# Kernel optimization log

Measured on AMD Instinct MI355X. Metric: run time of the kernel, lower is better.

## Reference

```python
import jax, jax.numpy as jnp
import numpy as np

N_EMBD = 128
N_HEADS = 8
HEAD_SIZE = N_EMBD // N_HEADS  # 16
EPS = 1e-5


def _layernorm(x, g, b):
    m = jnp.mean(x, axis=-1, keepdims=True)
    v = jnp.mean(jnp.square(x - m), axis=-1, keepdims=True)
    return (x - m) * jax.lax.rsqrt(v + EPS) * g + b


def setup_inputs() -> dict:
    key = jax.random.key(0)
    ks = jax.random.split(key, 12)
    B, T, D, H, HS = 16, 1024, N_EMBD, N_HEADS, HEAD_SIZE
    s = 1.0 / np.sqrt(D)
    inp = {
        "x": jax.random.normal(ks[0], (B, T, D), jnp.float32),
        # per-head QKV projections (stacked over heads; matches ModuleList of Linear(D, HS))
        "Wq": jax.random.uniform(ks[1], (H, D, HS), jnp.float32, -s, s),
        "bq": jnp.zeros((H, HS), jnp.float32),
        "Wk": jax.random.uniform(ks[2], (H, D, HS), jnp.float32, -s, s),
        "bk": jnp.zeros((H, HS), jnp.float32),
        "Wv": jax.random.uniform(ks[3], (H, D, HS), jnp.float32, -s, s),
        "bv": jnp.zeros((H, HS), jnp.float32),
        "Wp": jax.random.uniform(ks[4], (H * HS, D), jnp.float32, -s, s),
        "bp": jnp.zeros((D,), jnp.float32),
        "W1": jax.random.uniform(ks[5], (D, 4 * D), jnp.float32, -s, s),
        "b1": jnp.zeros((4 * D,), jnp.float32),
        "W2": jax.random.uniform(ks[6], (4 * D, D), jnp.float32, -1.0 / np.sqrt(4 * D), 1.0 / np.sqrt(4 * D)),
        "b2": jnp.zeros((D,), jnp.float32),
        "g1": jnp.ones((D,), jnp.float32),
        "be1": jnp.zeros((D,), jnp.float32),
        "g2": jnp.ones((D,), jnp.float32),
        "be2": jnp.zeros((D,), jnp.float32),
    }
    return inp


def reference(x, Wq, bq, Wk, bk, Wv, bv, Wp, bp, W1, b1, W2, b2, g1, be1, g2, be2):
    B, T, D = x.shape
    # batched per-head projections: [B,T,D] x [H,D,HS] -> [B,H,T,HS]
    q = jnp.einsum("btd,hds->bhts", x, Wq) + bq[None, :, None, :]
    k = jnp.einsum("btd,hds->bhts", x, Wk) + bk[None, :, None, :]
    v = jnp.einsum("btd,hds->bhts", x, Wv) + bv[None, :, None, :]
    scores = jnp.einsum("bhts,bhus->bhtu", q, k) / np.sqrt(HEAD_SIZE).astype(np.float32)
    tril = jnp.tril(jnp.ones((T, T), x.dtype))
    # faithful to source: multiplicative + additive mask (not -inf where)
    scores = scores * tril - 1e12 * (1.0 - tril)
    attn = jax.nn.softmax(scores, axis=-1)
    out = jnp.einsum("bhtu,bhus->bhts", attn, v)  # [B,H,T,HS]
    # concat heads in head order -> [B,T,H*HS]
    out = out.transpose(0, 2, 1, 3).reshape(B, T, -1)
    attn_out = out @ Wp + bp
    x = _layernorm(attn_out + x, g1, be1)
    h = jax.nn.gelu(x @ W1 + b1, approximate=False) @ W2 + b2
    x = _layernorm(h + x, g2, be2)
    return x
```

## Files before the change

### kernel.cpp

```cpp
#include <hip/hip_runtime.h>
#include <hip/hip_bf16.h>
#include <math.h>

constexpr int NB  = 16;
constexpr int NT  = 1024;
constexpr int ND  = 128;
constexpr int NH  = 8;
constexpr int NHS = 16;
constexpr int NDH = 512;
constexpr long NBT = (long)NB * NT;

typedef __attribute__((ext_vector_type(8))) short short8;
typedef __attribute__((ext_vector_type(4))) float f32x4;
typedef __attribute__((ext_vector_type(4))) unsigned short us4;

__device__ __forceinline__ unsigned short f2bf(float f) {
    __hip_bfloat16 h = __float2bfloat16(f);
    return *(unsigned short*)&h;
}

__device__ __forceinline__ short8 cvt8(const float* p) {
    const float4 f0 = *(const float4*)p;
    const float4 f1 = *(const float4*)(p + 4);
    union { short8 s; __hip_bfloat162 h[4]; } u;
    u.h[0] = __float22bfloat162_rn(make_float2(f0.x, f0.y));
    u.h[1] = __float22bfloat162_rn(make_float2(f0.z, f0.w));
    u.h[2] = __float22bfloat162_rn(make_float2(f1.x, f1.y));
    u.h[3] = __float22bfloat162_rn(make_float2(f1.z, f1.w));
    return u.s;
}

__device__ __forceinline__ float fast_gelu(float y) {
    const float t = y * y;
    const float u = __builtin_fmaf(y * 0.044715f, t, y);
    const float e = __builtin_amdgcn_exp2f(u * -2.302118131f);
    return y * __builtin_amdgcn_rcpf(1.0f + e);
}

__global__ __launch_bounds__(256) void k_prep(
    const float* __restrict__ Wq, const float* __restrict__ Wk,
    const float* __restrict__ Wv, __hip_bfloat16* __restrict__ Wqkvt)
{
    const int blk = blockIdx.x, tid = threadIdx.x;
    const int i0 = blk * 1024 + tid * 4;
    const int n = i0 >> 7, d0 = i0 & 127;
    const int sec = n >> 7, m = n & 127;
    const float* W = (sec == 0) ? Wq : (sec == 1) ? Wk : Wv;
    const float* src = W + (m >> 4) * 2048 + (m & 15);
    us4 v;
    #pragma unroll
    for (int j = 0; j < 4; ++j) v[j] = f2bf(src[(d0 + j) * 16]);
    *(us4*)((unsigned short*)Wqkvt + i0) = v;
}

__global__ __launch_bounds__(256) void k_qkv(
    const float* __restrict__ x, const __hip_bfloat16* __restrict__ Wqkvt,
    const float* __restrict__ bq, const float* __restrict__ bk,
    const float* __restrict__ bv,
    const float* __restrict__ Wp, const float* __restrict__ W1,
    const float* __restrict__ W2,
    __hip_bfloat16* __restrict__ Wpt, __hip_bfloat16* __restrict__ W1t,
    __hip_bfloat16* __restrict__ W2t,
    __hip_bfloat16* __restrict__ qo, __hip_bfloat16* __restrict__ ko,
    __hip_bfloat16* __restrict__ vo)
{
    __shared__ __align__(16) unsigned short st[32 * 392];
    const int tid = threadIdx.x;

    if (blockIdx.x >= 512) {
        const int blk = blockIdx.x - 512 + 48;
        us4 v;
        if (blk < 64) {
            const int i0 = (blk - 48) * 1024 + tid * 4;
            const int n = i0 >> 7, d0 = i0 & 127;
            #pragma unroll
            for (int j = 0; j < 4; ++j) v[j] = f2bf(Wp[(d0 + j) * 128 + n]);
            *(us4*)((unsigned short*)Wpt + i0) = v;
        } else if (blk < 128) {
            const int i0 = (blk - 64) * 1024 + tid * 4;
            const int n = i0 >> 7, d0 = i0 & 127;
            #pragma unroll
            for (int j = 0; j < 4; ++j) v[j] = f2bf(W1[(d0 + j) * 512 + n]);
            *(us4*)((unsigned short*)W1t + i0) = v;
        } else {
            const int i0 = (blk - 128) * 1024 + tid * 4;
            const int n = i0 >> 9, k0 = i0 & 511;
            #pragma unroll
            for (int j = 0; j < 4; ++j) v[j] = f2bf(W2[(k0 + j) * 128 + n]);
            *(us4*)((unsigned short*)W2t + i0) = v;
        }
        return;
    }

    const int w    = tid >> 6;
    const int lane = tid & 63;
    const int sL   = lane & 15;
    const int quad = lane >> 4;
    const int tok0 = blockIdx.x * 32;

    const unsigned short* W = (const unsigned short*)Wqkvt;

    short8 bx[2][4];
    #pragma unroll
    for (int tt = 0; tt < 2; ++tt)
        #pragma unroll
        for (int ks = 0; ks < 4; ++ks)
            bx[tt][ks] = cvt8(x + (size_t)(tok0 + tt * 16 + sL) * 128 + ks * 32 + quad * 8);

    f32x4 acc[6][2];
    #pragma unroll
    for (int ci = 0; ci < 6; ++ci)
        #pragma unroll
        for (int tt = 0; tt < 2; ++tt)
            acc[ci][tt] = (f32x4){0.f, 0.f, 0.f, 0.f};

    #pragma unroll
    for (int ks = 0; ks < 4; ++ks) {
        short8 aW[6];
        #pragma unroll
        for (int ci = 0; ci < 6; ++ci) {
            const int ct = w * 6 + ci;
            aW[ci] = *(const short8*)(W + (size_t)(ct * 16 + sL) * 128 + ks * 32 + quad * 8);
        }
        #pragma unroll
        for (int ci = 0; ci < 6; ++ci)
            #pragma unroll
            for (int tt = 0; tt < 2; ++tt)
                acc[ci][tt] = __builtin_amdgcn_mfma_f32_16x16x32_bf16(aW[ci], bx[tt][ks], acc[ci][tt], 0, 0, 0);
    }

    const float qscale = 0.3606737602f;
    #pragma unroll
    for (int ci = 0; ci < 6; ++ci) {
        const int ct = w * 6 + ci;
        const int kind = ct >> 3;
        const int ncc = (ct & 7) * 16 + quad * 4;
        const float4 bb = *(const float4*)(((kind == 0) ? bq : (kind == 1) ? bk : bv) + ncc);
        #pragma unroll
        for (int tt = 0; tt < 2; ++tt) {
            us4 v;
            #pragma unroll
            for (int r = 0; r < 4; ++r) {
                float val = acc[ci][tt][r] + ((const float*)&bb)[r];
                if (kind == 0) val *= qscale;
                v[r] = f2bf(val);
            }
            *(us4*)(st + (tt * 16 + sL) * 392 + ct * 16 + quad * 4) = v;
        }
    }
    __syncthreads();

    const int b = tok0 >> 10, tt0 = tok0 & 1023;
    {
        const int h = tid >> 5, tok = tid & 31;
        const unsigned short* sq = st + tok * 392 + h * 16;
        const unsigned short* sk = st + tok * 392 + 128 + h * 16;
        unsigned short* dq = (unsigned short*)qo + ((size_t)(b * 8 + h) * 1024 + tt0 + tok) * 16;
        unsigned short* dk = (unsigned short*)ko + ((size_t)(b * 8 + h) * 1024 + tt0 + tok) * 16;
        *(short8*)dq       = *(const short8*)sq;
        *(short8*)(dq + 8) = *(const short8*)(sq + 8);
        *(short8*)dk       = *(const short8*)sk;
        *(short8*)(dk + 8) = *(const short8*)(sk + 8);
    }
    if (tid < 128) {
        const int h = tid >> 4, s = tid & 15;
        unsigned short tmp[32];
        #pragma unroll
        for (int tok = 0; tok < 32; ++tok)
            tmp[tok] = st[tok * 392 + 256 + h * 16 + s];
        unsigned short* dv = (unsigned short*)vo + ((size_t)(b * 8 + h) * 16 + s) * 1024 + tt0;
        #pragma unroll
        for (int j = 0; j < 4; ++j)
            *(short8*)(dv + j * 8) = *(const short8*)(tmp + j * 8);
    }
}

__global__ __launch_bounds__(256) void k_attn(
    const __hip_bfloat16* __restrict__ qb, const __hip_bfloat16* __restrict__ kb,
    const __hip_bfloat16* __restrict__ vtb, __hip_bfloat16* __restrict__ att)
{
    const int bh   = blockIdx.x & 127;
    const int sub  = blockIdx.x >> 7;
    const int wave = threadIdx.x >> 6;
    const int lane = threadIdx.x & 63;
    const int sL   = lane & 15;
    const int q    = lane >> 4;
    const int b = bh >> 3, h = bh & 7;
    const int tile = sub * 4 + wave;

    const char* qbase = (const char*)qb  + (size_t)bh * NT * NHS * 2;
    const char* kbase = (const char*)kb  + (size_t)bh * NT * NHS * 2;
    const char* vbase = (const char*)vtb + (size_t)bh * NHS * NT * 2;

    const short8 zz = {0,0,0,0,0,0,0,0};

    const int t0 = tile * 16;
    const int tmy = t0 + sL;

    short8 bQ = zz;
    if (q < 2) bQ = *(const short8*)(qbase + (size_t)tmy * 32 + q * 16);

    f32x4 o = {0.f, 0.f, 0.f, 0.f};
    float lp = 0.f;

    const int nch = (t0 + 47) >> 5;
    for (int c = 0; c < nch; ++c) {
        const int u0 = c * 32;
        short8 aK0 = zz, aK1 = zz;
        if (q < 2) {
            aK0 = *(const short8*)(kbase + (size_t)(u0 + sL) * 32 + q * 16);
            aK1 = *(const short8*)(kbase + (size_t)(u0 + 16 + sL) * 32 + q * 16);
        }
        const f32x4 zc = {0.f, 0.f, 0.f, 0.f};
        f32x4 sT0 = __builtin_amdgcn_mfma_f32_16x16x32_bf16(aK0, bQ, zc, 0, 0, 0);
        f32x4 sT1 = __builtin_amdgcn_mfma_f32_16x16x32_bf16(aK1, bQ, zc, 0, 0, 0);

        int pk[4];
        if (u0 + 31 <= t0) {
            #pragma unroll
            for (int r = 0; r < 4; ++r) {
                const float p0 = __builtin_amdgcn_exp2f(sT0[r]);
                const float p1 = __builtin_amdgcn_exp2f(sT1[r]);
                lp += p0 + p1;
                __hip_bfloat162 hh = __float22bfloat162_rn(make_float2(p0, p1));
                pk[r] = *(int*)&hh;
            }
        } else {
            #pragma unroll
            for (int r = 0; r < 4; ++r) {
                const int ua = u0 + 4 * q + r;
                const float e0 = __builtin_amdgcn_exp2f(sT0[r]);
                const float e1 = __builtin_amdgcn_exp2f(sT1[r]);
                const float p0 = (ua      <= tmy) ? e0 : 0.f;
                const float p1 = (ua + 16 <= tmy) ? e1 : 0.f;
                lp += p0 + p1;
                __hip_bfloat162 hh = __float22bfloat162_rn(make_float2(p0, p1));
                pk[r] = *(int*)&hh;
            }
        }

        short8 bP;
        #pragma unroll
        for (int j = 0; j < 8; ++j) {
            const int srcq = ((q & 1) << 1) + (j >> 2);
            const int src  = (srcq << 4) + sL;
            const int g = __shfl(pk[j & 3], src);
            bP[j] = (short)((q < 2) ? (g & 0xffff) : ((unsigned)g >> 16));
        }

        const short8 aV = *(const short8*)(vbase + ((size_t)sL * NT + u0 + q * 8) * 2);
        o = __builtin_amdgcn_mfma_f32_16x16x32_bf16(aV, bP, o, 0, 0, 0);
    }

    float l = lp;
    l += __shfl_xor(l, 16);
    l += __shfl_xor(l, 32);
    const float inv = 1.0f / l;
    us4 res;
    res[0] = f2bf(o[0] * inv); res[1] = f2bf(o[1] * inv);
    res[2] = f2bf(o[2] * inv); res[3] = f2bf(o[3] * inv);
    *(us4*)((unsigned short*)att + ((size_t)b * NT + tmy) * ND + h * NHS + q * 4) = res;
}

__global__ __launch_bounds__(256) void k_tail(
    const __hip_bfloat16* __restrict__ attb, const __hip_bfloat16* __restrict__ Wpt,
    const __hip_bfloat16* __restrict__ W1t, const __hip_bfloat16* __restrict__ W2t,
    const float* __restrict__ x, const float* __restrict__ bp,
    const float* __restrict__ g1, const float* __restrict__ be1,
    const float* __restrict__ b1, const float* __restrict__ b2,
    const float* __restrict__ g2, const float* __restrict__ be2,
    float* __restrict__ out)
{
    __shared__ float ys[32][132];
    __shared__ __align__(16) unsigned short l1b[32 * 136];
    __shared__ __align__(16) unsigned short midb[32 * 528];
    const int w    = threadIdx.x >> 6;
    const int lane = threadIdx.x & 63;
    const int sL   = lane & 15;
    const int quad = lane >> 4;
    const int tok0 = blockIdx.x * 32;

    {
        const unsigned short* A = (const unsigned short*)attb;
        const unsigned short* W = (const unsigned short*)Wpt;
        short8 bfr[2][4];
        #pragma unroll
        for (int tt = 0; tt < 2; ++tt)
            #pragma unroll
            for (int ks = 0; ks < 4; ++ks)
                bfr[tt][ks] = *(const short8*)(A + (size_t)(tok0 + tt * 16 + sL) * 128 + ks * 32 + quad * 8);

        f32x4 acc[2][2];
        #pragma unroll
        for (int ci = 0; ci < 2; ++ci)
            #pragma unroll
            for (int tt = 0; tt < 2; ++tt)
                acc[ci][tt] = (f32x4){0.f, 0.f, 0.f, 0.f};

        #pragma unroll
        for (int ks = 0; ks < 4; ++ks) {
            short8 aW[2];
            #pragma unroll
            for (int ci = 0; ci < 2; ++ci)
                aW[ci] = *(const short8*)(W + (size_t)((w * 2 + ci) * 16 + sL) * 128 + ks * 32 + quad * 8);
            #pragma unroll
            for (int ci = 0; ci < 2; ++ci)
                #pragma unroll
                for (int tt = 0; tt < 2; ++tt)
                    acc[ci][tt] = __builtin_amdgcn_mfma_f32_16x16x32_bf16(aW[ci], bfr[tt][ks], acc[ci][tt], 0, 0, 0);
        }
        #pragma unroll
        for (int ci = 0; ci < 2; ++ci) {
            const int n0 = (w * 2 + ci) * 16 + quad * 4;
            const float4 bb = *(const float4*)(bp + n0);
            #pragma unroll
            for (int tt = 0; tt < 2; ++tt) {
                float4 v;
                v.x = acc[ci][tt][0] + bb.x; v.y = acc[ci][tt][1] + bb.y;
                v.z = acc[ci][tt][2] + bb.z; v.w = acc[ci][tt][3] + bb.w;
                *(float4*)(&ys[tt * 16 + sL][n0]) = v;
            }
        }
    }
    __syncthreads();

    const int tok = threadIdx.x >> 3;
    const int l8  = threadIdx.x & 7;
    const int c0  = l8 * 16;
    {
        float vals[16];
        float s = 0.f, s2 = 0.f;
        #pragma unroll
        for (int ch = 0; ch < 4; ++ch) {
            const float4 ly = *(const float4*)&ys[tok][c0 + ch * 4];
            const float4 gx = *(const float4*)(x + (size_t)(tok0 + tok) * 128 + c0 + ch * 4);
            vals[ch*4+0] = ly.x + gx.x; vals[ch*4+1] = ly.y + gx.y;
            vals[ch*4+2] = ly.z + gx.z; vals[ch*4+3] = ly.w + gx.w;
            #pragma unroll
            for (int j = 0; j < 4; ++j) { s += vals[ch*4+j]; s2 += vals[ch*4+j] * vals[ch*4+j]; }
        }
        #pragma unroll
        for (int off = 1; off <= 4; off <<= 1) {
            s  += __shfl_xor(s, off, 8);
            s2 += __shfl_xor(s2, off, 8);
        }
        const float mean = s * (1.0f / 128.0f);
        const float var  = s2 * (1.0f / 128.0f) - mean * mean;
        const float rstd = rsqrtf(var + 1e-5f);
        #pragma unroll
        for (int ch = 0; ch < 4; ++ch) {
            const float4 gg = *(const float4*)(g1 + c0 + ch * 4);
            const float4 bb = *(const float4*)(be1 + c0 + ch * 4);
            float ln0 = (vals[ch*4+0] - mean) * rstd * gg.x + bb.x;
            float ln1v = (vals[ch*4+1] - mean) * rstd * gg.y + bb.y;
            float ln2v = (vals[ch*4+2] - mean) * rstd * gg.z + bb.z;
            float ln3 = (vals[ch*4+3] - mean) * rstd * gg.w + bb.w;
            ys[tok][c0 + ch*4 + 0] = ln0;
            ys[tok][c0 + ch*4 + 1] = ln1v;
            ys[tok][c0 + ch*4 + 2] = ln2v;
            ys[tok][c0 + ch*4 + 3] = ln3;
            us4 lb;
            lb[0] = f2bf(ln0); lb[1] = f2bf(ln1v); lb[2] = f2bf(ln2v); lb[3] = f2bf(ln3);
            *(us4*)(l1b + tok * 136 + c0 + ch * 4) = lb;
        }
    }
    __syncthreads();

    {
        const unsigned short* W = (const unsigned short*)W1t;
        short8 bl[2][4];
        #pragma unroll
        for (int tt = 0; tt < 2; ++tt)
            #pragma unroll
            for (int ks = 0; ks < 4; ++ks)
                bl[tt][ks] = *(const short8*)(l1b + (tt * 16 + sL) * 136 + ks * 32 + quad * 8);

        f32x4 acc[8][2];
        #pragma unroll
        for (int ci = 0; ci < 8; ++ci)
            #pragma unroll
            for (int tt = 0; tt < 2; ++tt)
                acc[ci][tt] = (f32x4){0.f, 0.f, 0.f, 0.f};

        #pragma unroll
        for (int ks = 0; ks < 4; ++ks) {
            short8 aW[8];
            #pragma unroll
            for (int ci = 0; ci < 8; ++ci)
                aW[ci] = *(const short8*)(W + (size_t)((w * 8 + ci) * 16 + sL) * 128 + ks * 32 + quad * 8);
            #pragma unroll
            for (int ci = 0; ci < 8; ++ci)
                #pragma unroll
                for (int tt = 0; tt < 2; ++tt)
                    acc[ci][tt] = __builtin_amdgcn_mfma_f32_16x16x32_bf16(aW[ci], bl[tt][ks], acc[ci][tt], 0, 0, 0);
        }
        #pragma unroll
        for (int ci = 0; ci < 8; ++ci) {
            const int n0 = (w * 8 + ci) * 16 + quad * 4;
            const float4 bb = *(const float4*)(b1 + n0);
            #pragma unroll
            for (int tt = 0; tt < 2; ++tt) {
                us4 v;
                v[0] = f2bf(fast_gelu(acc[ci][tt][0] + bb.x));
                v[1] = f2bf(fast_gelu(acc[ci][tt][1] + bb.y));
                v[2] = f2bf(fast_gelu(acc[ci][tt][2] + bb.z));
                v[3] = f2bf(fast_gelu(acc[ci][tt][3] + bb.w));
                *(us4*)(midb + (tt * 16 + sL) * 528 + n0) = v;
            }
        }
    }
    __syncthreads();

    f32x4 acc2[2][2];
    #pragma unroll
    for (int ci = 0; ci < 2; ++ci)
        #pragma unroll
        for (int tt = 0; tt < 2; ++tt)
            acc2[ci][tt] = (f32x4){0.f, 0.f, 0.f, 0.f};
    {
        const unsigned short* W = (const unsigned short*)W2t;
        #pragma unroll
        for (int ks = 0; ks < 16; ++ks) {
            short8 bm0 = *(const short8*)(midb + (size_t)sL * 528 + ks * 32 + quad * 8);
            short8 bm1 = *(const short8*)(midb + (size_t)(16 + sL) * 528 + ks * 32 + quad * 8);
            short8 aW0 = *(const short8*)(W + (size_t)((w * 2) * 16 + sL) * 512 + ks * 32 + quad * 8);
            short8 aW1 = *(const short8*)(W + (size_t)((w * 2 + 1) * 16 + sL) * 512 + ks * 32 + quad * 8);
            acc2[0][0] = __builtin_amdgcn_mfma_f32_16x16x32_bf16(aW0, bm0, acc2[0][0], 0, 0, 0);
            acc2[0][1] = __builtin_amdgcn_mfma_f32_16x16x32_bf16(aW0, bm1, acc2[0][1], 0, 0, 0);
            acc2[1][0] = __builtin_amdgcn_mfma_f32_16x16x32_bf16(aW1, bm0, acc2[1][0], 0, 0, 0);
            acc2[1][1] = __builtin_amdgcn_mfma_f32_16x16x32_bf16(aW1, bm1, acc2[1][1], 0, 0, 0);
        }
    }
    __syncthreads();
    float* ys2 = (float*)midb;
    #pragma unroll
    for (int ci = 0; ci < 2; ++ci) {
        const int n0 = (w * 2 + ci) * 16 + quad * 4;
        const float4 bb = *(const float4*)(b2 + n0);
        #pragma unroll
        for (int tt = 0; tt < 2; ++tt) {
            float4 v;
            v.x = acc2[ci][tt][0] + bb.x; v.y = acc2[ci][tt][1] + bb.y;
            v.z = acc2[ci][tt][2] + bb.z; v.w = acc2[ci][tt][3] + bb.w;
            *(float4*)(ys2 + (tt * 16 + sL) * 132 + n0) = v;
        }
    }
    __syncthreads();

    {
        float vals[16];
        float s = 0.f, s2 = 0.f;
        #pragma unroll
        for (int ch = 0; ch < 4; ++ch) {
            const float4 ly = *(const float4*)(ys2 + tok * 132 + c0 + ch * 4);
            const float4 gx = *(const float4*)&ys[tok][c0 + ch * 4];
            vals[ch*4+0] = ly.x + gx.x; vals[ch*4+1] = ly.y + gx.y;
            vals[ch*4+2] = ly.z + gx.z; vals[ch*4+3] = ly.w + gx.w;
            #pragma unroll
            for (int j = 0; j < 4; ++j) { s += vals[ch*4+j]; s2 += vals[ch*4+j] * vals[ch*4+j]; }
        }
        #pragma unroll
        for (int off = 1; off <= 4; off <<= 1) {
            s  += __shfl_xor(s, off, 8);
            s2 += __shfl_xor(s2, off, 8);
        }
        const float mean = s * (1.0f / 128.0f);
        const float var  = s2 * (1.0f / 128.0f) - mean * mean;
        const float rstd = rsqrtf(var + 1e-5f);
        #pragma unroll
        for (int ch = 0; ch < 4; ++ch) {
            const float4 gg = *(const float4*)(g2 + c0 + ch * 4);
            const float4 bb = *(const float4*)(be2 + c0 + ch * 4);
            float4 ln;
            ln.x = (vals[ch*4+0] - mean) * rstd * gg.x + bb.x;
            ln.y = (vals[ch*4+1] - mean) * rstd * gg.y + bb.y;
            ln.z = (vals[ch*4+2] - mean) * rstd * gg.z + bb.z;
            ln.w = (vals[ch*4+3] - mean) * rstd * gg.w + bb.w;
            *(float4*)(out + (size_t)(tok0 + tok) * 128 + c0 + ch * 4) = ln;
        }
    }
}

extern "C" void kernel_launch(void* const* d_in, const int* in_sizes, int n_in,
                              void* d_out, int out_size, void* d_ws, size_t ws_size,
                              hipStream_t stream)
{
    (void)in_sizes; (void)n_in; (void)out_size; (void)ws_size;
    const float* x   = (const float*)d_in[0];
    const float* Wq  = (const float*)d_in[1];
    const float* bq  = (const float*)d_in[2];
    const float* Wk  = (const float*)d_in[3];
    const float* bk  = (const float*)d_in[4];
    const float* Wv  = (const float*)d_in[5];
    const float* bv  = (const float*)d_in[6];
    const float* Wp  = (const float*)d_in[7];
    const float* bp  = (const float*)d_in[8];
    const float* W1  = (const float*)d_in[9];
    const float* b1  = (const float*)d_in[10];
    const float* W2  = (const float*)d_in[11];
    const float* b2  = (const float*)d_in[12];
    const float* g1  = (const float*)d_in[13];
    const float* be1 = (const float*)d_in[14];
    const float* g2  = (const float*)d_in[15];
    const float* be2 = (const float*)d_in[16];
    float* out = (float*)d_out;

    char* wsb = (char*)d_ws;
    __hip_bfloat16* qb   = (__hip_bfloat16*)wsb;
    __hip_bfloat16* kb   = (__hip_bfloat16*)(wsb + (4u  << 20));
    __hip_bfloat16* vtb  = (__hip_bfloat16*)(wsb + (8u  << 20));
    __hip_bfloat16* attb = (__hip_bfloat16*)(wsb + (12u << 20));
    __hip_bfloat16* Wqkvt= (__hip_bfloat16*)(wsb + (16u << 20));
    __hip_bfloat16* Wpt  = (__hip_bfloat16*)(wsb + (16u << 20) + (96u  << 10));
    __hip_bfloat16* W1t  = (__hip_bfloat16*)(wsb + (16u << 20) + (128u << 10));
    __hip_bfloat16* W2t  = (__hip_bfloat16*)(wsb + (16u << 20) + (256u << 10));

    k_prep<<<48,   256, 0, stream>>>(Wq, Wk, Wv, Wqkvt);
    k_qkv <<<656,  256, 0, stream>>>(x, Wqkvt, bq, bk, bv, Wp, W1, W2,
                                     Wpt, W1t, W2t, qb, kb, vtb);
    k_attn<<<2048, 256, 0, stream>>>(qb, kb, vtb, attb);
    k_tail<<<512,  256, 0, stream>>>(attb, Wpt, W1t, W2t, x, bp, g1, be1,
                                     b1, b2, g2, be2, out);
}
```

Baseline: 163.6 us.

## Halve tail kernel token tile to 16 and rebalance causal attention tile mapping

The tail kernel now processes 16 tokens per block instead of 32, doubling the grid to 1024 blocks and shrinking shared memory and accumulator registers. This gives more blocks across the CUs and higher occupancy. The cost is that each block reloads the same weight fragments for half as many tokens, doubling weight traffic from L2. Separately, attention tiles are now assigned as wave*16+sub, so each block mixes short and long causal rows, which is meant to even out per-block work.

```diff
diff --git a/kernel.cpp b/kernel.cpp
--- a/kernel.cpp
+++ b/kernel.cpp
@@ -186,7 +186,7 @@
     const int sL   = lane & 15;
     const int q    = lane >> 4;
     const int b = bh >> 3, h = bh & 7;
-    const int tile = sub * 4 + wave;
+    const int tile = wave * 16 + sub;
 
     const char* qbase = (const char*)qb  + (size_t)bh * NT * NHS * 2;
     const char* kbase = (const char*)kb  + (size_t)bh * NT * NHS * 2;
@@ -271,67 +271,55 @@
     const float* __restrict__ g2, const float* __restrict__ be2,
     float* __restrict__ out)
 {
-    __shared__ float ys[32][132];
-    __shared__ __align__(16) unsigned short l1b[32 * 136];
-    __shared__ __align__(16) unsigned short midb[32 * 528];
+    __shared__ float ys[16][132];
+    __shared__ __align__(16) unsigned short l1b[16 * 136];
+    __shared__ __align__(16) unsigned short midb[16 * 528];
     const int w    = threadIdx.x >> 6;
     const int lane = threadIdx.x & 63;
     const int sL   = lane & 15;
     const int quad = lane >> 4;
-    const int tok0 = blockIdx.x * 32;
+    const int tok0 = blockIdx.x * 16;
 
     {
         const unsigned short* A = (const unsigned short*)attb;
         const unsigned short* W = (const unsigned short*)Wpt;
-        short8 bfr[2][4];
-        #pragma unroll
-        for (int tt = 0; tt < 2; ++tt)
-            #pragma unroll
-            for (int ks = 0; ks < 4; ++ks)
-                bfr[tt][ks] = *(const short8*)(A + (size_t)(tok0 + tt * 16 + sL) * 128 + ks * 32 + quad * 8);
-
-        f32x4 acc[2][2];
-        #pragma unroll
-        for (int ci = 0; ci < 2; ++ci)
-            #pragma unroll
-            for (int tt = 0; tt < 2; ++tt)
-                acc[ci][tt] = (f32x4){0.f, 0.f, 0.f, 0.f};
+        short8 bfr[4];
+        #pragma unroll
+        for (int ks = 0; ks < 4; ++ks)
+            bfr[ks] = *(const short8*)(A + (size_t)(tok0 + sL) * 128 + ks * 32 + quad * 8);
+
+        f32x4 acc[2];
+        acc[0] = (f32x4){0.f, 0.f, 0.f, 0.f};
+        acc[1] = (f32x4){0.f, 0.f, 0.f, 0.f};
 
         #pragma unroll
         for (int ks = 0; ks < 4; ++ks) {
-            short8 aW[2];
-            #pragma unroll
-            for (int ci = 0; ci < 2; ++ci)
-                aW[ci] = *(const short8*)(W + (size_t)((w * 2 + ci) * 16 + sL) * 128 + ks * 32 + quad * 8);
-            #pragma unroll
-            for (int ci = 0; ci < 2; ++ci)
-                #pragma unroll
-                for (int tt = 0; tt < 2; ++tt)
-                    acc[ci][tt] = __builtin_amdgcn_mfma_f32_16x16x32_bf16(aW[ci], bfr[tt][ks], acc[ci][tt], 0, 0, 0);
+            #pragma unroll
+            for (int ci = 0; ci < 2; ++ci) {
+                const short8 aW = *(const short8*)(W + (size_t)((w * 2 + ci) * 16 + sL) * 128 + ks * 32 + quad * 8);
+                acc[ci] = __builtin_amdgcn_mfma_f32_16x16x32_bf16(aW, bfr[ks], acc[ci], 0, 0, 0);
+            }
         }
         #pragma unroll
         for (int ci = 0; ci < 2; ++ci) {
             const int n0 = (w * 2 + ci) * 16 + quad * 4;
             const float4 bb = *(const float4*)(bp + n0);
-            #pragma unroll
-            for (int tt = 0; tt < 2; ++tt) {
-                float4 v;
-                v.x = acc[ci][tt][0] + bb.x; v.y = acc[ci][tt][1] + bb.y;
-                v.z = acc[ci][tt][2] + bb.z; v.w = acc[ci][tt][3] + bb.w;
-                *(float4*)(&ys[tt * 16 + sL][n0]) = v;
-            }
-        }
-    }
-    __syncthreads();
-
-    const int tok = threadIdx.x >> 3;
-    const int l8  = threadIdx.x & 7;
-    const int c0  = l8 * 16;
-    {
-        float vals[16];
+            float4 v;
+            v.x = acc[ci][0] + bb.x; v.y = acc[ci][1] + bb.y;
+            v.z = acc[ci][2] + bb.z; v.w = acc[ci][3] + bb.w;
+            *(float4*)(&ys[sL][n0]) = v;
+        }
+    }
+    __syncthreads();
+
+    const int tok = threadIdx.x >> 4;
+    const int l16 = threadIdx.x & 15;
+    const int c0  = l16 * 8;
+    {
+        float vals[8];
         float s = 0.f, s2 = 0.f;
         #pragma unroll
-        for (int ch = 0; ch < 4; ++ch) {
+        for (int ch = 0; ch < 2; ++ch) {
             const float4 ly = *(const float4*)&ys[tok][c0 + ch * 4];
             const float4 gx = *(const float4*)(x + (size_t)(tok0 + tok) * 128 + c0 + ch * 4);
             vals[ch*4+0] = ly.x + gx.x; vals[ch*4+1] = ly.y + gx.y;
@@ -340,15 +328,15 @@
             for (int j = 0; j < 4; ++j) { s += vals[ch*4+j]; s2 += vals[ch*4+j] * vals[ch*4+j]; }
         }
         #pragma unroll
-        for (int off = 1; off <= 4; off <<= 1) {
-            s  += __shfl_xor(s, off, 8);
-            s2 += __shfl_xor(s2, off, 8);
+        for (int off = 1; off <= 8; off <<= 1) {
+            s  += __shfl_xor(s, off, 16);
+            s2 += __shfl_xor(s2, off, 16);
         }
         const float mean = s * (1.0f / 128.0f);
         const float var  = s2 * (1.0f / 128.0f) - mean * mean;
         const float rstd = rsqrtf(var + 1e-5f);
         #pragma unroll
-        for (int ch = 0; ch < 4; ++ch) {
+        for (int ch = 0; ch < 2; ++ch) {
             const float4 gg = *(const float4*)(g1 + c0 + ch * 4);
             const float4 bb = *(const float4*)(be1 + c0 + ch * 4);
             float ln0 = (vals[ch*4+0] - mean) * rstd * gg.x + bb.x;
@@ -368,67 +356,50 @@
 
     {
         const unsigned short* W = (const unsigned short*)W1t;
-        short8 bl[2][4];
-        #pragma unroll
-        for (int tt = 0; tt < 2; ++tt)
-            #pragma unroll
-            for (int ks = 0; ks < 4; ++ks)
-                bl[tt][ks] = *(const short8*)(l1b + (tt * 16 + sL) * 136 + ks * 32 + quad * 8);
-
-        f32x4 acc[8][2];
+        short8 bl[4];
+        #pragma unroll
+        for (int ks = 0; ks < 4; ++ks)
+            bl[ks] = *(const short8*)(l1b + sL * 136 + ks * 32 + quad * 8);
+
+        f32x4 acc[8];
         #pragma unroll
         for (int ci = 0; ci < 8; ++ci)
-            #pragma unroll
-            for (int tt = 0; tt < 2; ++tt)
-                acc[ci][tt] = (f32x4){0.f, 0.f, 0.f, 0.f};
+            acc[ci] = (f32x4){0.f, 0.f, 0.f, 0.f};
 
         #pragma unroll
         for (int ks = 0; ks < 4; ++ks) {
-            short8 aW[8];
-            #pragma unroll
-            for (int ci = 0; ci < 8; ++ci)
-                aW[ci] = *(const short8*)(W + (size_t)((w * 8 + ci) * 16 + sL) * 128 + ks * 32 + quad * 8);
-            #pragma unroll
-            for (int ci = 0; ci < 8; ++ci)
-                #pragma unroll
-                for (int tt = 0; tt < 2; ++tt)
-                    acc[ci][tt] = __builtin_amdgcn_mfma_f32_16x16x32_bf16(aW[ci], bl[tt][ks], acc[ci][tt], 0, 0, 0);
+            #pragma unroll
+            for (int ci = 0; ci < 8; ++ci) {
+                const short8 aW = *(const short8*)(W + (size_t)((w * 8 + ci) * 16 + sL) * 128 + ks * 32 + quad * 8);
+                acc[ci] = __builtin_amdgcn_mfma_f32_16x16x32_bf16(aW, bl[ks], acc[ci], 0, 0, 0);
+            }
         }
         #pragma unroll
         for (int ci = 0; ci < 8; ++ci) {
             const int n0 = (w * 8 + ci) * 16 + quad * 4;
             const float4 bb = *(const float4*)(b1 + n0);
-            #pragma unroll
-            for (int tt = 0; tt < 2; ++tt) {
-                us4 v;
-                v[0] = f2bf(fast_gelu(acc[ci][tt][0] + bb.x));
-                v[1] = f2bf(fast_gelu(acc[ci][tt][1] + bb.y));
-                v[2] = f2bf(fast_gelu(acc[ci][tt][2] + bb.z));
-                v[3] = f2bf(fast_gelu(acc[ci][tt][3] + bb.w));
-                *(us4*)(midb + (tt * 16 + sL) * 528 + n0) = v;
-            }
-        }
-    }
-    __syncthreads();
-
-    f32x4 acc2[2][2];
-    #pragma unroll
-    for (int ci = 0; ci < 2; ++ci)
-        #pragma unroll
-        for (int tt = 0; tt < 2; ++tt)
-            acc2[ci][tt] = (f32x4){0.f, 0.f, 0.f, 0.f};
+            us4 v;
+            v[0] = f2bf(fast_gelu(acc[ci][0] + bb.x));
+            v[1] = f2bf(fast_gelu(acc[ci][1] + bb.y));
+            v[2] = f2bf(fast_gelu(acc[ci][2] + bb.z));
+            v[3] = f2bf(fast_gelu(acc[ci][3] + bb.w));
+            *(us4*)(midb + sL * 528 + n0) = v;
+        }
+    }
+    __syncthreads();
+
+    f32x4 acc2[2];
+    acc2[0] = (f32x4){0.f, 0.f, 0.f, 0.f};
+    acc2[1] = (f32x4){0.f, 0.f, 0.f, 0.f};
     {
         const unsigned short* W = (const unsigned short*)W2t;
         #pragma unroll
         for (int ks = 0; ks < 16; ++ks) {
-            short8 bm0 = *(const short8*)(midb + (size_t)sL * 528 + ks * 32 + quad * 8);
-            short8 bm1 = *(const short8*)(midb + (size_t)(16 + sL) * 528 + ks * 32 + quad * 8);
-            short8 aW0 = *(const short8*)(W + (size_t)((w * 2) * 16 + sL) * 512 + ks * 32 + quad * 8);
-            short8 aW1 = *(const short8*)(W + (size_t)((w * 2 + 1) * 16 + sL) * 512 + ks * 32 + quad * 8);
-            acc2[0][0] = __builtin_amdgcn_mfma_f32_16x16x32_bf16(aW0, bm0, acc2[0][0], 0, 0, 0);
-            acc2[0][1] = __builtin_amdgcn_mfma_f32_16x16x32_bf16(aW0, bm1, acc2[0][1], 0, 0, 0);
-            acc2[1][0] = __builtin_amdgcn_mfma_f32_16x16x32_bf16(aW1, bm0, acc2[1][0], 0, 0, 0);
-            acc2[1][1] = __builtin_amdgcn_mfma_f32_16x16x32_bf16(aW1, bm1, acc2[1][1], 0, 0, 0);
+            const short8 bm = *(const short8*)(midb + (size_t)sL * 528 + ks * 32 + quad * 8);
+            const short8 aW0 = *(const short8*)(W + (size_t)((w * 2) * 16 + sL) * 512 + ks * 32 + quad * 8);
+            const short8 aW1 = *(const short8*)(W + (size_t)((w * 2 + 1) * 16 + sL) * 512 + ks * 32 + quad * 8);
+            acc2[0] = __builtin_amdgcn_mfma_f32_16x16x32_bf16(aW0, bm, acc2[0], 0, 0, 0);
+            acc2[1] = __builtin_amdgcn_mfma_f32_16x16x32_bf16(aW1, bm, acc2[1], 0, 0, 0);
         }
     }
     __syncthreads();
@@ -437,21 +408,18 @@
     for (int ci = 0; ci < 2; ++ci) {
         const int n0 = (w * 2 + ci) * 16 + quad * 4;
         const float4 bb = *(const float4*)(b2 + n0);
-        #pragma unroll
-        for (int tt = 0; tt < 2; ++tt) {
-            float4 v;
-            v.x = acc2[ci][tt][0] + bb.x; v.y = acc2[ci][tt][1] + bb.y;
-            v.z = acc2[ci][tt][2] + bb.z; v.w = acc2[ci][tt][3] + bb.w;
-            *(float4*)(ys2 + (tt * 16 + sL) * 132 + n0) = v;
-        }
-    }
-    __syncthreads();
-
-    {
-        float vals[16];
+        float4 v;
+        v.x = acc2[ci][0] + bb.x; v.y = acc2[ci][1] + bb.y;
+        v.z = acc2[ci][2] + bb.z; v.w = acc2[ci][3] + bb.w;
+        *(float4*)(ys2 + sL * 132 + n0) = v;
+    }
+    __syncthreads();
+
+    {
+        float vals[8];
         float s = 0.f, s2 = 0.f;
         #pragma unroll
-        for (int ch = 0; ch < 4; ++ch) {
+        for (int ch = 0; ch < 2; ++ch) {
             const float4 ly = *(const float4*)(ys2 + tok * 132 + c0 + ch * 4);
             const float4 gx = *(const float4*)&ys[tok][c0 + ch * 4];
             vals[ch*4+0] = ly.x + gx.x; vals[ch*4+1] = ly.y + gx.y;
@@ -460,15 +428,15 @@
             for (int j = 0; j < 4; ++j) { s += vals[ch*4+j]; s2 += vals[ch*4+j] * vals[ch*4+j]; }
         }
         #pragma unroll
-        for (int off = 1; off <= 4; off <<= 1) {
-            s  += __shfl_xor(s, off, 8);
-            s2 += __shfl_xor(s2, off, 8);
+        for (int off = 1; off <= 8; off <<= 1) {
+            s  += __shfl_xor(s, off, 16);
+            s2 += __shfl_xor(s2, off, 16);
         }
         const float mean = s * (1.0f / 128.0f);
         const float var  = s2 * (1.0f / 128.0f) - mean * mean;
         const float rstd = rsqrtf(var + 1e-5f);
         #pragma unroll
-        for (int ch = 0; ch < 4; ++ch) {
+        for (int ch = 0; ch < 2; ++ch) {
             const float4 gg = *(const float4*)(g2 + c0 + ch * 4);
             const float4 bb = *(const float4*)(be2 + c0 + ch * 4);
             float4 ln;
@@ -519,6 +487,6 @@
     k_qkv <<<656,  256, 0, stream>>>(x, Wqkvt, bq, bk, bv, Wp, W1, W2,
                                      Wpt, W1t, W2t, qb, kb, vtb);
     k_attn<<<2048, 256, 0, stream>>>(qb, kb, vtb, attb);
-    k_tail<<<512,  256, 0, stream>>>(attb, Wpt, W1t, W2t, x, bp, g1, be1,
+    k_tail<<<1024, 256, 0, stream>>>(attb, Wpt, W1t, W2t, x, bp, g1, be1,
                                      b1, b2, g2, be2, out);
 }
```

After: 175.7 us. 1.07x slower.
